# Kernel tuning notes

Hardware: AMD Instinct MI355X
Metric: run time of the kernel (lower is better)

## Reference

```python
import jax, jax.numpy as jnp
import numpy as np

B, F, U, A, H = 8192, 1024, 256, 16, 8  # batch, in_features, units_layer, num_actions, hidden(=8)


def _coagent_layer(x, W0, b0, W1, b1, W2, b2):
    # x: [B, f_in]; stacked weights for U independent tiny MLPs (grouped GEMMs)
    h = jax.nn.relu(jnp.einsum('bf,uhf->buh', x, W0) + b0)   # [B, U, H]
    h = jax.nn.relu(jnp.einsum('buh,ugh->bug', h, W1) + b1)  # [B, U, H]
    q = jnp.einsum('bug,uag->bua', h, W2) + b2               # [B, U, A]
    # greedy action per coagent (epsilon-greedy with greedy=True / epsilon=0)
    return jnp.argmax(q, axis=-1).astype(jnp.float32)        # [B, U]


def setup_inputs() -> dict:
    key = jax.random.key(0)
    ks = jax.random.split(key, 19)
    n = lambda k, shape, fan: (jax.random.normal(k, shape, dtype=jnp.float32)
                               / jnp.sqrt(jnp.float32(fan)))
    return {
        'state': jax.random.normal(ks[0], (B, F), dtype=jnp.float32),
        # coagent layer 0: in_features -> 8 -> 8 -> A, stacked over U units
        'W0_0': n(ks[1], (U, H, F), F), 'b0_0': jnp.zeros((U, H), jnp.float32),
        'W1_0': n(ks[2], (U, H, H), H), 'b1_0': jnp.zeros((U, H), jnp.float32),
        'W2_0': n(ks[3], (U, A, H), H), 'b2_0': jnp.zeros((U, A), jnp.float32),
        # coagent layer 1: units_layer -> 8 -> 8 -> A, stacked over U units
        'W0_1': n(ks[4], (U, H, U), U), 'b0_1': jnp.zeros((U, H), jnp.float32),
        'W1_1': n(ks[5], (U, H, H), H), 'b1_1': jnp.zeros((U, H), jnp.float32),
        'W2_1': n(ks[6], (U, A, H), H), 'b2_1': jnp.zeros((U, A), jnp.float32),
        # Policy head: units_layer -> 8 -> 8 -> 1
        'PW0': n(ks[7], (H, U), U), 'Pb0': jnp.zeros((H,), jnp.float32),
        'PW1': n(ks[8], (H, H), H), 'Pb1': jnp.zeros((H,), jnp.float32),
        'PW2': n(ks[9], (1, H), H), 'Pb2': jnp.zeros((1,), jnp.float32),
    }


def reference(state, W0_0, b0_0, W1_0, b1_0, W2_0, b2_0,
              W0_1, b0_1, W1_1, b1_1, W2_1, b2_1,
              PW0, Pb0, PW1, Pb1, PW2, Pb2):
    a0 = _coagent_layer(state, W0_0, b0_0, W1_0, b1_0, W2_0, b2_0)  # [B, U]
    a1 = _coagent_layer(a0, W0_1, b0_1, W1_1, b1_1, W2_1, b2_1)     # [B, U]
    h = jax.nn.relu(a1 @ PW0.T + Pb0)
    h = jax.nn.relu(h @ PW1.T + Pb1)
    return h @ PW2.T + Pb2  # [B, 1]
```

## Files before the change

### kernel.cpp

```cpp
#include <hip/hip_runtime.h>
#include <cstring>
#include <cstdint>

#define B_TOTAL 8192
#define F_IN    1024
#define U_UNITS 256
#define NACT    16
#define HID     8

typedef float    f32x4  __attribute__((ext_vector_type(4)));
typedef _Float16 half8  __attribute__((ext_vector_type(8)));
typedef _Float16 half4  __attribute__((ext_vector_type(4)));


__device__ __forceinline__ void gload_lds16(const _Float16* g, _Float16* l)
{
    __builtin_amdgcn_global_load_lds(
        (const __attribute__((address_space(1))) void*)g,
        (__attribute__((address_space(3))) void*)l,
        16, 0, 0);
}

__global__ __launch_bounds__(256)
void pack3_kernel(const float* __restrict__ s0, _Float16* __restrict__ d0h, _Float16* __restrict__ d0l,
                  const float* __restrict__ s1, _Float16* __restrict__ d1h, _Float16* __restrict__ d1l,
                  const float* __restrict__ s2, _Float16* __restrict__ d2h, _Float16* __restrict__ d2l)
{
    constexpr int NB0 = (B_TOTAL / 16) * (F_IN / 128);
    constexpr int NB1 = (U_UNITS * HID / 16) * (F_IN / 128);
    __shared__ float ls[16 * 132];
    int b = blockIdx.x;
    const float* src; _Float16 *dh, *dl; int K, lg;
    if (b < NB0)            { src = s0; dh = d0h; dl = d0l; K = F_IN;    lg = 3; }
    else if (b < NB0 + NB1) { b -= NB0; src = s1; dh = d1h; dl = d1l; K = F_IN; lg = 3; }
    else                    { b -= NB0 + NB1; src = s2; dh = d2h; dl = d2l; K = U_UNITS; lg = 1; }

    const int tid = threadIdx.x;
    const int mt  = b >> lg;
    const int kb  = b & ((1 << lg) - 1);
    const int r0  = mt * 16;

#pragma unroll
    for (int i = 0; i < 2; ++i) {
        const int e = tid + (i << 8);
        const int row = e >> 5;
        const int c4  = e & 31;
        f32x4 v = *reinterpret_cast<const f32x4*>(
            &src[(size_t)(r0 + row) * K + (kb << 7) + (c4 << 2)]);
        *reinterpret_cast<f32x4*>(&ls[row * 132 + (c4 << 2)]) = v;
    }
    __syncthreads();

    const int k8 = tid >> 4, r = tid & 15;
    float x[8];
#pragma unroll
    for (int j = 0; j < 8; ++j) x[j] = ls[r * 132 + (k8 << 3) + j];
    half8 h, l;
#pragma unroll
    for (int j = 0; j < 8; ++j) {
        h[j] = (_Float16)x[j];
        l[j] = (_Float16)((x[j] - (float)h[j]) * 2048.0f);
    }
    const size_t off = (((size_t)mt * (K >> 5)) + (kb << 2) + (k8 >> 2)) * 512
                     + (size_t)(((k8 & 3) << 4) + r) * 8;
    *reinterpret_cast<half8*>(&dh[off]) = h;
    *reinterpret_cast<half8*>(&dl[off]) = l;
}

constexpr int BM = 128, BN = 128;

template<int K_TOTAL, bool A_SPLIT, bool OUT_TF32>
__global__ __launch_bounds__(256, 2)
void coagent_mfma(const _Float16* __restrict__ Ahg, const _Float16* __restrict__ Alg,
                  const _Float16* __restrict__ Bhg, const _Float16* __restrict__ Blg,
                  const float* __restrict__ b0, const float* __restrict__ W1,
                  const float* __restrict__ b1, const float* __restrict__ W2,
                  const float* __restrict__ b2, void* __restrict__ outp)
{
    struct EpiBufs { float Hs[BM][65]; _Float16 ab[BM * 8]; };
    union SMemU { _Float16 stage[2][16384]; EpiBufs epi; };
    __shared__ SMemU sm;

    constexpr int NTK = K_TOTAL >> 5;
    constexpr size_t TS = (size_t)NTK * 512;

    const int tid  = threadIdx.x;
    const int wave = tid >> 6;
    const int lane = tid & 63;
    const int quad = lane >> 4;
    const int l15  = lane & 15;
    const int wm   = (wave >> 1) * 64;

    const int flat = blockIdx.y * 16 + blockIdx.x;
    const int vid  = (flat & 7) * 128 + (flat >> 3);
    const int m0   = (vid & 63) * BM;
    const int n0   = (vid >> 6) * BN;

    const int at = (wave >> 1) * 4;
    const int bt = (wave & 1) * 4;

    const _Float16* greg = Ahg; int tb = m0 >> 4;
    if (wave == 1)      { greg = A_SPLIT ? Alg : Ahg; }
    else if (wave == 2) { greg = Bhg; tb = n0 >> 4; }
    else if (wave == 3) { greg = Blg; tb = n0 >> 4; }
    const _Float16* gbase = greg + (size_t)tb * TS + lane * 8;

    f32x4 acc1[4][4];
    f32x4 acc2[4][4];
#pragma unroll
    for (int i = 0; i < 4; ++i)
#pragma unroll
        for (int j = 0; j < 4; ++j) { acc1[i][j] = {0.f,0.f,0.f,0.f}; acc2[i][j] = {0.f,0.f,0.f,0.f}; }

    if (A_SPLIT || wave != 1) {
#pragma unroll
        for (int i = 0; i < 8; ++i)
            gload_lds16(gbase + (size_t)i * TS, &sm.stage[0][(wave * 8 + i) * 512]);
    }
    __syncthreads();

    int cur = 0;
#pragma unroll 1
    for (int kt = 0; kt < NTK; ++kt) {
        if (kt + 1 < NTK && (A_SPLIT || wave != 1)) {
            const _Float16* g = gbase + (size_t)(kt + 1) * 512;
#pragma unroll
            for (int i = 0; i < 8; ++i)
                gload_lds16(g + (size_t)i * TS, &sm.stage[cur ^ 1][(wave * 8 + i) * 512]);
        }

        const _Float16* SB = sm.stage[cur];
        half8 af[4], bf[4], la[4], lb[4];
#pragma unroll
        for (int mt = 0; mt < 4; ++mt)
            af[mt] = *reinterpret_cast<const half8*>(&SB[(at + mt) * 512 + lane * 8]);
#pragma unroll
        for (int nt = 0; nt < 4; ++nt)
            bf[nt] = *reinterpret_cast<const half8*>(&SB[8192 + (bt + nt) * 512 + lane * 8]);
        if constexpr (A_SPLIT) {
#pragma unroll
            for (int mt = 0; mt < 4; ++mt)
                la[mt] = *reinterpret_cast<const half8*>(&SB[4096 + (at + mt) * 512 + lane * 8]);
        }
#pragma unroll
        for (int nt = 0; nt < 4; ++nt)
            lb[nt] = *reinterpret_cast<const half8*>(&SB[12288 + (bt + nt) * 512 + lane * 8]);

#pragma unroll
        for (int mt = 0; mt < 4; ++mt)
#pragma unroll
            for (int nt = 0; nt < 4; ++nt)
                acc1[mt][nt] = __builtin_amdgcn_mfma_f32_16x16x32_f16(af[mt], bf[nt], acc1[mt][nt], 0, 0, 0);
        if constexpr (A_SPLIT) {
#pragma unroll
            for (int mt = 0; mt < 4; ++mt)
#pragma unroll
                for (int nt = 0; nt < 4; ++nt)
                    acc2[mt][nt] = __builtin_amdgcn_mfma_f32_16x16x32_f16(la[mt], bf[nt], acc2[mt][nt], 0, 0, 0);
        }
#pragma unroll
        for (int mt = 0; mt < 4; ++mt)
#pragma unroll
            for (int nt = 0; nt < 4; ++nt)
                acc2[mt][nt] = __builtin_amdgcn_mfma_f32_16x16x32_f16(af[mt], lb[nt], acc2[mt][nt], 0, 0, 0);

        __syncthreads();
        cur ^= 1;
    }

    const int ubase = n0 >> 3;
    for (int half = 0; half < 2; ++half) {
        __syncthreads();
        if ((wave & 1) == half) {
#pragma unroll
            for (int mt = 0; mt < 4; ++mt)
#pragma unroll
                for (int nt = 0; nt < 4; ++nt)
#pragma unroll
                    for (int r = 0; r < 4; ++r)
                        sm.epi.Hs[wm + mt * 16 + quad * 4 + r][nt * 16 + l15] =
                            acc1[mt][nt][r] + acc2[mt][nt][r] * (1.0f / 2048.0f);
        }
        __syncthreads();
#pragma unroll
        for (int p = 0; p < 4; ++p) {
            const int pair = (p << 8) + tid;
            const int ul = pair >> 7;
            const int bl = pair & 127;
            const int u  = __builtin_amdgcn_readfirstlane(ubase + half * 8 + ul);
            const float* __restrict__ b0u = b0 + u * 8;
            const float* __restrict__ W1u = W1 + u * 64;
            const float* __restrict__ b1u = b1 + u * 8;
            const float* __restrict__ W2u = W2 + u * 128;
            const float* __restrict__ b2u = b2 + u * 16;

            float h[HID];
#pragma unroll
            for (int j = 0; j < HID; ++j)
                h[j] = fmaxf(sm.epi.Hs[bl][ul * 8 + j] + b0u[j], 0.f);

            float h2[HID];
#pragma unroll
            for (int g = 0; g < HID; ++g) {
                float s = b1u[g];
#pragma unroll
                for (int j = 0; j < HID; ++j)
                    s += h[j] * W1u[g * 8 + j];
                h2[g] = fmaxf(s, 0.f);
            }

            float best = b2u[0];
#pragma unroll
            for (int j = 0; j < HID; ++j) best += h2[j] * W2u[j];
            int bi = 0;
#pragma unroll
            for (int a = 1; a < NACT; ++a) {
                float s = b2u[a];
#pragma unroll
                for (int j = 0; j < HID; ++j)
                    s += h2[j] * W2u[a * 8 + j];
                if (s > best) { best = s; bi = a; }
            }

            if (OUT_TF32) {
                ((float*)outp)[(size_t)u * B_TOTAL + m0 + bl] = (float)bi;
            } else {
                sm.epi.ab[bl * 8 + ul] = (_Float16)bi;
            }
        }
        if (!OUT_TF32) {
            __syncthreads();
            if (tid < 128) {
                float4 v = *reinterpret_cast<float4*>(&sm.epi.ab[tid * 8]);
                const int u = ubase + half * 8;
                const int b = m0 + tid;
                const size_t off = ((size_t)(b >> 4) * 8 + (u >> 5)) * 512
                                 + (size_t)((((u >> 3) & 3) << 4) + (b & 15)) * 8;
                *reinterpret_cast<float4*>(&((_Float16*)outp)[off]) = v;
            }
        }
    }
}


constexpr int FBM = 128, FBN = 128, FBK = 16;

template<int K_TOTAL, bool X_TRANSPOSED>
__global__ __launch_bounds__(256, 2)
void coagent_kernel(const float* __restrict__ X, const float* __restrict__ W0,
                    const float* __restrict__ b0, const float* __restrict__ W1,
                    const float* __restrict__ b1, const float* __restrict__ W2,
                    const float* __restrict__ b2, float* __restrict__ outT)
{
    struct SMemGemm { float As[FBK][FBM + 4]; float Bs[FBK][FBN + 4]; };
    union SMem { SMemGemm g; float Hs[FBM][65]; };
    __shared__ SMem sm;

    const int tid = threadIdx.x;
    const int tx = tid & 15, ty = tid >> 4;
    const int m0 = blockIdx.y * FBM, n0 = blockIdx.x * FBN;

    float acc[8][8];
#pragma unroll
    for (int i = 0; i < 8; ++i)
#pragma unroll
        for (int j = 0; j < 8; ++j) acc[i][j] = 0.f;

    for (int k0 = 0; k0 < K_TOTAL; k0 += FBK) {
        __syncthreads();
        if (X_TRANSPOSED) {
#pragma unroll
            for (int l = tid; l < (FBM * FBK) / 4; l += 256) {
                const int k = l >> 5, q = l & 31;
                const float4 v = *reinterpret_cast<const float4*>(
                    &X[(size_t)(k0 + k) * B_TOTAL + m0 + 4 * q]);
                *reinterpret_cast<float4*>(&sm.g.As[k][4 * q]) = v;
            }
        } else {
#pragma unroll
            for (int l = tid; l < (FBM * FBK) / 4; l += 256) {
                const int row = l >> 2, c = l & 3;
                const float4 v = *reinterpret_cast<const float4*>(
                    &X[(size_t)(m0 + row) * K_TOTAL + k0 + 4 * c]);
                sm.g.As[4 * c + 0][row] = v.x; sm.g.As[4 * c + 1][row] = v.y;
                sm.g.As[4 * c + 2][row] = v.z; sm.g.As[4 * c + 3][row] = v.w;
            }
        }
#pragma unroll
        for (int l = tid; l < (FBN * FBK) / 4; l += 256) {
            const int row = l >> 2, c = l & 3;
            const float4 v = *reinterpret_cast<const float4*>(
                &W0[(size_t)(n0 + row) * K_TOTAL + k0 + 4 * c]);
            sm.g.Bs[4 * c + 0][row] = v.x; sm.g.Bs[4 * c + 1][row] = v.y;
            sm.g.Bs[4 * c + 2][row] = v.z; sm.g.Bs[4 * c + 3][row] = v.w;
        }
        __syncthreads();
#pragma unroll
        for (int k = 0; k < FBK; ++k) {
            float a[8], bb[8];
            *reinterpret_cast<float4*>(&a[0])  = *reinterpret_cast<float4*>(&sm.g.As[k][4 * ty]);
            *reinterpret_cast<float4*>(&a[4])  = *reinterpret_cast<float4*>(&sm.g.As[k][64 + 4 * ty]);
            *reinterpret_cast<float4*>(&bb[0]) = *reinterpret_cast<float4*>(&sm.g.Bs[k][4 * tx]);
            *reinterpret_cast<float4*>(&bb[4]) = *reinterpret_cast<float4*>(&sm.g.Bs[k][64 + 4 * tx]);
#pragma unroll
            for (int i = 0; i < 8; ++i)
#pragma unroll
                for (int j = 0; j < 8; ++j) acc[i][j] += a[i] * bb[j];
        }
    }

    const int ub_base = n0 >> 3;
    for (int half = 0; half < 2; ++half) {
        __syncthreads();
#pragma unroll
        for (int i = 0; i < 8; ++i) {
            const int row = (i < 4) ? (4 * ty + i) : (64 + 4 * ty + (i - 4));
#pragma unroll
            for (int j = 0; j < 4; ++j)
                sm.Hs[row][4 * tx + j] = acc[i][4 * half + j];
        }
        __syncthreads();
#pragma unroll
        for (int p = 0; p < 4; ++p) {
            const int pair = (p << 8) + tid;
            const int ul = pair >> 7, bl = pair & 127;
            const int u = ub_base + half * 8 + ul;
            float h[HID];
#pragma unroll
            for (int j = 0; j < HID; ++j)
                h[j] = fmaxf(sm.Hs[bl][ul * 8 + j] + b0[u * 8 + j], 0.f);
            float h2[HID];
#pragma unroll
            for (int g = 0; g < HID; ++g) {
                float s = b1[u * 8 + g];
#pragma unroll
                for (int j = 0; j < HID; ++j) s += h[j] * W1[u * 64 + g * 8 + j];
                h2[g] = fmaxf(s, 0.f);
            }
            float best = b2[u * 16];
#pragma unroll
            for (int j = 0; j < HID; ++j) best += h2[j] * W2[u * 128 + j];
            int bi = 0;
#pragma unroll
            for (int a = 1; a < NACT; ++a) {
                float s = b2[u * 16 + a];
#pragma unroll
                for (int j = 0; j < HID; ++j) s += h2[j] * W2[u * 128 + a * 8 + j];
                if (s > best) { best = s; bi = a; }
            }
            outT[(size_t)u * B_TOTAL + m0 + bl] = (float)bi;
        }
    }
}

__global__ __launch_bounds__(256)
void policy_kernel(const float* __restrict__ A1T,
                   const float* __restrict__ PW0, const float* __restrict__ Pb0,
                   const float* __restrict__ PW1, const float* __restrict__ Pb1,
                   const float* __restrict__ PW2, const float* __restrict__ Pb2,
                   float* __restrict__ out)
{
    __shared__ float part[8][32][HID + 1];
    const int tid = threadIdx.x;
    const int b32 = tid & 31;
    const int sl  = tid >> 5;
    const int b   = blockIdx.x * 32 + b32;

    float hp[HID];
#pragma unroll
    for (int j = 0; j < HID; ++j) hp[j] = 0.f;

#pragma unroll 1
    for (int q0 = 0; q0 < 32; q0 += 8) {
        float v[8];
#pragma unroll
        for (int t = 0; t < 8; ++t)
            v[t] = A1T[(size_t)(sl * 32 + q0 + t) * B_TOTAL + b];
#pragma unroll
        for (int t = 0; t < 8; ++t)
#pragma unroll
            for (int j = 0; j < HID; ++j)
                hp[j] += v[t] * PW0[j * U_UNITS + sl * 32 + q0 + t];
    }
#pragma unroll
    for (int j = 0; j < HID; ++j) part[sl][b32][j] = hp[j];
    __syncthreads();

    if (sl == 0) {
        float h[HID];
#pragma unroll
        for (int j = 0; j < HID; ++j) {
            float s = Pb0[j];
#pragma unroll
            for (int s8 = 0; s8 < 8; ++s8) s += part[s8][b32][j];
            h[j] = fmaxf(s, 0.f);
        }
        float h2[HID];
#pragma unroll
        for (int g = 0; g < HID; ++g) {
            float s = Pb1[g];
#pragma unroll
            for (int j = 0; j < HID; ++j) s += h[j] * PW1[g * 8 + j];
            h2[g] = fmaxf(s, 0.f);
        }
        float o = Pb2[0];
#pragma unroll
        for (int j = 0; j < HID; ++j) o += h2[j] * PW2[j];
        out[b] = o;
    }
}


extern "C" void kernel_launch(void* const* d_in, const int* in_sizes, int n_in,
                              void* d_out, int out_size, void* d_ws, size_t ws_size,
                              hipStream_t stream)
{
    const float* state = (const float*)d_in[0];
    const float* W0_0  = (const float*)d_in[1];
    const float* b0_0  = (const float*)d_in[2];
    const float* W1_0  = (const float*)d_in[3];
    const float* b1_0  = (const float*)d_in[4];
    const float* W2_0  = (const float*)d_in[5];
    const float* b2_0  = (const float*)d_in[6];
    const float* W0_1  = (const float*)d_in[7];
    const float* b0_1  = (const float*)d_in[8];
    const float* W1_1  = (const float*)d_in[9];
    const float* b1_1  = (const float*)d_in[10];
    const float* W2_1  = (const float*)d_in[11];
    const float* b2_1  = (const float*)d_in[12];
    const float* PW0   = (const float*)d_in[13];
    const float* Pb0   = (const float*)d_in[14];
    const float* PW1   = (const float*)d_in[15];
    const float* Pb1   = (const float*)d_in[16];
    const float* PW2   = (const float*)d_in[17];
    const float* Pb2   = (const float*)d_in[18];

    const size_t SZ_STATE = (size_t)B_TOTAL * F_IN;
    const size_t SZ_W00   = (size_t)U_UNITS * HID * F_IN;
    const size_t SZ_W01   = (size_t)U_UNITS * HID * U_UNITS;
    const size_t NEED = (2 * SZ_STATE + 2 * SZ_W00 + 2 * SZ_W01
                         + (size_t)B_TOTAL * U_UNITS) * 2
                        + (size_t)U_UNITS * B_TOTAL * 4;

    if (ws_size >= NEED) {
        char* p = (char*)d_ws;
        _Float16* state_h = (_Float16*)p;                p += SZ_STATE * 2;
        _Float16* state_l = (_Float16*)p;                p += SZ_STATE * 2;
        _Float16* w00_h   = (_Float16*)p;                p += SZ_W00 * 2;
        _Float16* w00_l   = (_Float16*)p;                p += SZ_W00 * 2;
        _Float16* w01_h   = (_Float16*)p;                p += SZ_W01 * 2;
        _Float16* w01_l   = (_Float16*)p;                p += SZ_W01 * 2;
        _Float16* a0      = (_Float16*)p;                p += (size_t)B_TOTAL * U_UNITS * 2;
        float*    a1T     = (float*)p;

        constexpr int NB0 = (B_TOTAL / 16) * (F_IN / 128);
        constexpr int NB1 = (U_UNITS * HID / 16) * (F_IN / 128);
        constexpr int NB2 = (U_UNITS * HID / 16) * (U_UNITS / 128);
        pack3_kernel<<<NB0 + NB1 + NB2, 256, 0, stream>>>(
            state, state_h, state_l, W0_0, w00_h, w00_l, W0_1, w01_h, w01_l);

        dim3 grid((U_UNITS * HID) / BN, B_TOTAL / BM);

        coagent_mfma<F_IN, true, false><<<grid, 256, 0, stream>>>(
            state_h, state_l, w00_h, w00_l, b0_0, W1_0, b1_0, W2_0, b2_0, (void*)a0);

        coagent_mfma<U_UNITS, false, true><<<grid, 256, 0, stream>>>(
            a0, nullptr, w01_h, w01_l, b0_1, W1_1, b1_1, W2_1, b2_1, (void*)a1T);

        policy_kernel<<<B_TOTAL / 32, 256, 0, stream>>>(
            a1T, PW0, Pb0, PW1, Pb1, PW2, Pb2, (float*)d_out);
    } else {
        float* a0T = (float*)d_ws;
        float* a1T = a0T + (size_t)U_UNITS * B_TOTAL;
        dim3 grid((U_UNITS * HID) / FBN, B_TOTAL / FBM);
        coagent_kernel<F_IN, false><<<grid, 256, 0, stream>>>(
            state, W0_0, b0_0, W1_0, b1_0, W2_0, b2_0, a0T);
        coagent_kernel<U_UNITS, true><<<grid, 256, 0, stream>>>(
            a0T, W0_1, b0_1, W1_1, b1_1, W2_1, b2_1, a1T);
        policy_kernel<<<B_TOTAL / 32, 256, 0, stream>>>(
            a1T, PW0, Pb0, PW1, Pb1, PW2, Pb2, (float*)d_out);
    }
}
```

Measured before the change: 319.5 us.

## Shrink MFMA coagent tile to 128x64 and raise occupancy to four blocks

Halves the N tile of the split-fp16 MFMA coagent GEMM from 128 to 64 and sizes the LDS staging buffer to what each variant needs. The accumulators shrink, so launch bounds allow four blocks per CU. The loader is rewritten so every wave issues an even share of the global-to-LDS chunks, where before one wave sat idle in the non-split case. The epilogue becomes a single pass over 8 units instead of two halves. This trades less B-operand reuse and more A reloads across N tiles for better latency hiding. It also drops the swizzled block-index mapping, which may change L2 locality.

```diff
diff --git a/kernel.cpp b/kernel.cpp
--- a/kernel.cpp
+++ b/kernel.cpp
@@ -10,7 +10,6 @@
 
 typedef float    f32x4  __attribute__((ext_vector_type(4)));
 typedef _Float16 half8  __attribute__((ext_vector_type(8)));
-typedef _Float16 half4  __attribute__((ext_vector_type(4)));
 
 
 __device__ __forceinline__ void gload_lds16(const _Float16* g, _Float16* l)
@@ -67,18 +66,23 @@
     *reinterpret_cast<half8*>(&dl[off]) = l;
 }
 
-constexpr int BM = 128, BN = 128;
+constexpr int BM = 128, BN = 64;
 
 template<int K_TOTAL, bool A_SPLIT, bool OUT_TF32>
-__global__ __launch_bounds__(256, 2)
+__global__ __launch_bounds__(256, 4)
 void coagent_mfma(const _Float16* __restrict__ Ahg, const _Float16* __restrict__ Alg,
                   const _Float16* __restrict__ Bhg, const _Float16* __restrict__ Blg,
                   const float* __restrict__ b0, const float* __restrict__ W1,
                   const float* __restrict__ b1, const float* __restrict__ W2,
                   const float* __restrict__ b2, void* __restrict__ outp)
 {
-    struct EpiBufs { float Hs[BM][65]; _Float16 ab[BM * 8]; };
-    union SMemU { _Float16 stage[2][16384]; EpiBufs epi; };
+    constexpr int BUFH  = A_SPLIT ? 12288 : 8192;
+    constexpr int BOFFH = A_SPLIT ? 8192 : 4096;
+    constexpr int BOFFL = A_SPLIT ? 10240 : 6144;
+    constexpr int NCH   = A_SPLIT ? 6 : 4;
+
+    struct EpiBufs { float Hs[BM][BN + 1]; _Float16 ab[BM * 8]; };
+    union SMemU { _Float16 stage[2][BUFH]; EpiBufs epi; };
     __shared__ SMemU sm;
 
     constexpr int NTK = K_TOTAL >> 5;
@@ -89,155 +93,153 @@
     const int lane = tid & 63;
     const int quad = lane >> 4;
     const int l15  = lane & 15;
-    const int wm   = (wave >> 1) * 64;
-
-    const int flat = blockIdx.y * 16 + blockIdx.x;
-    const int vid  = (flat & 7) * 128 + (flat >> 3);
-    const int m0   = (vid & 63) * BM;
-    const int n0   = (vid >> 6) * BN;
-
-    const int at = (wave >> 1) * 4;
-    const int bt = (wave & 1) * 4;
-
-    const _Float16* greg = Ahg; int tb = m0 >> 4;
-    if (wave == 1)      { greg = A_SPLIT ? Alg : Ahg; }
-    else if (wave == 2) { greg = Bhg; tb = n0 >> 4; }
-    else if (wave == 3) { greg = Blg; tb = n0 >> 4; }
-    const _Float16* gbase = greg + (size_t)tb * TS + lane * 8;
-
-    f32x4 acc1[4][4];
-    f32x4 acc2[4][4];
+
+    const int m0 = blockIdx.y * BM;
+    const int n0 = blockIdx.x * BN;
+
+    const int wmi = wave >> 1, wni = wave & 1;
+    const int at  = wmi * 4;
+    const int bt  = wni * 2;
+    const int wm  = wmi * 64, wn = wni * 32;
+
+    const _Float16* gs[NCH];
+#pragma unroll
+    for (int i = 0; i < NCH; ++i) {
+        const int c = wave * NCH + i;
+        const _Float16* base; int tile;
+        if (A_SPLIT) {
+            if (c < 8)       { base = Ahg; tile = (m0 >> 4) + c; }
+            else if (c < 16) { base = Alg; tile = (m0 >> 4) + (c - 8); }
+            else if (c < 20) { base = Bhg; tile = (n0 >> 4) + (c - 16); }
+            else             { base = Blg; tile = (n0 >> 4) + (c - 20); }
+        } else {
+            if (c < 8)       { base = Ahg; tile = (m0 >> 4) + c; }
+            else if (c < 12) { base = Bhg; tile = (n0 >> 4) + (c - 8); }
+            else             { base = Blg; tile = (n0 >> 4) + (c - 12); }
+        }
+        gs[i] = base + (size_t)tile * TS + lane * 8;
+    }
+
+    f32x4 acc1[4][2];
+    f32x4 acc2[4][2];
 #pragma unroll
     for (int i = 0; i < 4; ++i)
 #pragma unroll
-        for (int j = 0; j < 4; ++j) { acc1[i][j] = {0.f,0.f,0.f,0.f}; acc2[i][j] = {0.f,0.f,0.f,0.f}; }
-
-    if (A_SPLIT || wave != 1) {
-#pragma unroll
-        for (int i = 0; i < 8; ++i)
-            gload_lds16(gbase + (size_t)i * TS, &sm.stage[0][(wave * 8 + i) * 512]);
-    }
+        for (int j = 0; j < 2; ++j) { acc1[i][j] = {0.f,0.f,0.f,0.f}; acc2[i][j] = {0.f,0.f,0.f,0.f}; }
+
+#pragma unroll
+    for (int i = 0; i < NCH; ++i)
+        gload_lds16(gs[i], &sm.stage[0][(wave * NCH + i) * 512]);
     __syncthreads();
 
     int cur = 0;
 #pragma unroll 1
     for (int kt = 0; kt < NTK; ++kt) {
-        if (kt + 1 < NTK && (A_SPLIT || wave != 1)) {
-            const _Float16* g = gbase + (size_t)(kt + 1) * 512;
-#pragma unroll
-            for (int i = 0; i < 8; ++i)
-                gload_lds16(g + (size_t)i * TS, &sm.stage[cur ^ 1][(wave * 8 + i) * 512]);
-        }
-
-        const _Float16* SB = sm.stage[cur];
-        half8 af[4], bf[4], la[4], lb[4];
+        if (kt + 1 < NTK) {
+            _Float16* nb = &sm.stage[cur ^ 1][0];
+#pragma unroll
+            for (int i = 0; i < NCH; ++i)
+                gload_lds16(gs[i] + (size_t)(kt + 1) * 512, nb + (wave * NCH + i) * 512);
+        }
+
+        const _Float16* sb = &sm.stage[cur][0];
+        half8 af[4], la[4];
 #pragma unroll
         for (int mt = 0; mt < 4; ++mt)
-            af[mt] = *reinterpret_cast<const half8*>(&SB[(at + mt) * 512 + lane * 8]);
-#pragma unroll
-        for (int nt = 0; nt < 4; ++nt)
-            bf[nt] = *reinterpret_cast<const half8*>(&SB[8192 + (bt + nt) * 512 + lane * 8]);
+            af[mt] = *reinterpret_cast<const half8*>(&sb[(at + mt) * 512 + lane * 8]);
         if constexpr (A_SPLIT) {
 #pragma unroll
             for (int mt = 0; mt < 4; ++mt)
-                la[mt] = *reinterpret_cast<const half8*>(&SB[4096 + (at + mt) * 512 + lane * 8]);
-        }
-#pragma unroll
-        for (int nt = 0; nt < 4; ++nt)
-            lb[nt] = *reinterpret_cast<const half8*>(&SB[12288 + (bt + nt) * 512 + lane * 8]);
-
-#pragma unroll
-        for (int mt = 0; mt < 4; ++mt)
-#pragma unroll
-            for (int nt = 0; nt < 4; ++nt)
-                acc1[mt][nt] = __builtin_amdgcn_mfma_f32_16x16x32_f16(af[mt], bf[nt], acc1[mt][nt], 0, 0, 0);
-        if constexpr (A_SPLIT) {
+                la[mt] = *reinterpret_cast<const half8*>(&sb[4096 + (at + mt) * 512 + lane * 8]);
+        }
+
+#pragma unroll
+        for (int nt = 0; nt < 2; ++nt) {
+            half8 bf = *reinterpret_cast<const half8*>(&sb[BOFFH + (bt + nt) * 512 + lane * 8]);
+            half8 lb = *reinterpret_cast<const half8*>(&sb[BOFFL + (bt + nt) * 512 + lane * 8]);
 #pragma unroll
             for (int mt = 0; mt < 4; ++mt)
-#pragma unroll
-                for (int nt = 0; nt < 4; ++nt)
-                    acc2[mt][nt] = __builtin_amdgcn_mfma_f32_16x16x32_f16(la[mt], bf[nt], acc2[mt][nt], 0, 0, 0);
-        }
-#pragma unroll
-        for (int mt = 0; mt < 4; ++mt)
-#pragma unroll
-            for (int nt = 0; nt < 4; ++nt)
-                acc2[mt][nt] = __builtin_amdgcn_mfma_f32_16x16x32_f16(af[mt], lb[nt], acc2[mt][nt], 0, 0, 0);
+                acc1[mt][nt] = __builtin_amdgcn_mfma_f32_16x16x32_f16(af[mt], bf, acc1[mt][nt], 0, 0, 0);
+            if constexpr (A_SPLIT) {
+#pragma unroll
+                for (int mt = 0; mt < 4; ++mt)
+                    acc2[mt][nt] = __builtin_amdgcn_mfma_f32_16x16x32_f16(la[mt], bf, acc2[mt][nt], 0, 0, 0);
+            }
+#pragma unroll
+            for (int mt = 0; mt < 4; ++mt)
+                acc2[mt][nt] = __builtin_amdgcn_mfma_f32_16x16x32_f16(af[mt], lb, acc2[mt][nt], 0, 0, 0);
+        }
 
         __syncthreads();
         cur ^= 1;
     }
 
+#pragma unroll
+    for (int mt = 0; mt < 4; ++mt)
+#pragma unroll
+        for (int nt = 0; nt < 2; ++nt)
+#pragma unroll
+            for (int r = 0; r < 4; ++r)
+                sm.epi.Hs[wm + mt * 16 + quad * 4 + r][wn + nt * 16 + l15] =
+                    acc1[mt][nt][r] + acc2[mt][nt][r] * (1.0f / 2048.0f);
+    __syncthreads();
+
     const int ubase = n0 >> 3;
-    for (int half = 0; half < 2; ++half) {
-        __syncthreads();
-        if ((wave & 1) == half) {
-#pragma unroll
-            for (int mt = 0; mt < 4; ++mt)
-#pragma unroll
-                for (int nt = 0; nt < 4; ++nt)
-#pragma unroll
-                    for (int r = 0; r < 4; ++r)
-                        sm.epi.Hs[wm + mt * 16 + quad * 4 + r][nt * 16 + l15] =
-                            acc1[mt][nt][r] + acc2[mt][nt][r] * (1.0f / 2048.0f);
-        }
-        __syncthreads();
-#pragma unroll
-        for (int p = 0; p < 4; ++p) {
-            const int pair = (p << 8) + tid;
-            const int ul = pair >> 7;
-            const int bl = pair & 127;
-            const int u  = __builtin_amdgcn_readfirstlane(ubase + half * 8 + ul);
-            const float* __restrict__ b0u = b0 + u * 8;
-            const float* __restrict__ W1u = W1 + u * 64;
-            const float* __restrict__ b1u = b1 + u * 8;
-            const float* __restrict__ W2u = W2 + u * 128;
-            const float* __restrict__ b2u = b2 + u * 16;
-
-            float h[HID];
+#pragma unroll
+    for (int p = 0; p < 4; ++p) {
+        const int idx = (p << 8) + tid;
+        const int ul = idx >> 7;
+        const int bl = idx & 127;
+        const int u  = __builtin_amdgcn_readfirstlane(ubase + ul);
+        const float* __restrict__ b0u = b0 + u * 8;
+        const float* __restrict__ W1u = W1 + u * 64;
+        const float* __restrict__ b1u = b1 + u * 8;
+        const float* __restrict__ W2u = W2 + u * 128;
+        const float* __restrict__ b2u = b2 + u * 16;
+
+        float h[HID];
+#pragma unroll
+        for (int j = 0; j < HID; ++j)
+            h[j] = fmaxf(sm.epi.Hs[bl][ul * 8 + j] + b0u[j], 0.f);
+
+        float h2[HID];
+#pragma unroll
+        for (int g = 0; g < HID; ++g) {
+            float s = b1u[g];
 #pragma unroll
             for (int j = 0; j < HID; ++j)
-                h[j] = fmaxf(sm.epi.Hs[bl][ul * 8 + j] + b0u[j], 0.f);
-
-            float h2[HID];
-#pragma unroll
-            for (int g = 0; g < HID; ++g) {
-                float s = b1u[g];
-#pragma unroll
-                for (int j = 0; j < HID; ++j)
-                    s += h[j] * W1u[g * 8 + j];
-                h2[g] = fmaxf(s, 0.f);
-            }
-
-            float best = b2u[0];
-#pragma unroll
-            for (int j = 0; j < HID; ++j) best += h2[j] * W2u[j];
-            int bi = 0;
-#pragma unroll
-            for (int a = 1; a < NACT; ++a) {
-                float s = b2u[a];
-#pragma unroll
-                for (int j = 0; j < HID; ++j)
-                    s += h2[j] * W2u[a * 8 + j];
-                if (s > best) { best = s; bi = a; }
-            }
-
-            if (OUT_TF32) {
-                ((float*)outp)[(size_t)u * B_TOTAL + m0 + bl] = (float)bi;
-            } else {
-                sm.epi.ab[bl * 8 + ul] = (_Float16)bi;
-            }
-        }
-        if (!OUT_TF32) {
-            __syncthreads();
-            if (tid < 128) {
-                float4 v = *reinterpret_cast<float4*>(&sm.epi.ab[tid * 8]);
-                const int u = ubase + half * 8;
-                const int b = m0 + tid;
-                const size_t off = ((size_t)(b >> 4) * 8 + (u >> 5)) * 512
-                                 + (size_t)((((u >> 3) & 3) << 4) + (b & 15)) * 8;
-                *reinterpret_cast<float4*>(&((_Float16*)outp)[off]) = v;
-            }
+                s += h[j] * W1u[g * 8 + j];
+            h2[g] = fmaxf(s, 0.f);
+        }
+
+        float best = b2u[0];
+#pragma unroll
+        for (int j = 0; j < HID; ++j) best += h2[j] * W2u[j];
+        int bi = 0;
+#pragma unroll
+        for (int a = 1; a < NACT; ++a) {
+            float s = b2u[a];
+#pragma unroll
+            for (int j = 0; j < HID; ++j)
+                s += h2[j] * W2u[a * 8 + j];
+            if (s > best) { best = s; bi = a; }
+        }
+
+        if (OUT_TF32) {
+            ((float*)outp)[(size_t)u * B_TOTAL + m0 + bl] = (float)bi;
+        } else {
+            sm.epi.ab[bl * 8 + ul] = (_Float16)bi;
+        }
+    }
+    if (!OUT_TF32) {
+        __syncthreads();
+        if (tid < 128) {
+            float4 v = *reinterpret_cast<float4*>(&sm.epi.ab[tid * 8]);
+            const int u = ubase;
+            const int b = m0 + tid;
+            const size_t off = ((size_t)(b >> 4) * 8 + (u >> 5)) * 512
+                             + (size_t)((((u >> 3) & 3) << 4) + (b & 15)) * 8;
+            *reinterpret_cast<float4*>(&((_Float16*)outp)[off]) = v;
         }
     }
 }
```

Measured after the change: 281.9 us. 11.7% less time.
